# Optimization experiments

Hardware: AMD Instinct MI355X
Metric: run time of the kernel (lower is better)

The kernel has to match this reference:

```python
import jax, jax.numpy as jnp
import numpy as np

SEQ_LEN, BATCH, INPUT_SIZE, HIDDEN_SIZE = 512, 256, 256, 1024
ALPHA = 10.0 / 100.0  # dt / tau


def setup_inputs() -> dict:
    key = jax.random.key(0)
    k1, k2, k3, k4, k5 = jax.random.split(key, 5)
    s_in = 1.0 / np.sqrt(INPUT_SIZE)
    s_hh = 1.0 / np.sqrt(HIDDEN_SIZE)
    return {
        "x": jax.random.normal(k1, (SEQ_LEN, BATCH, INPUT_SIZE), jnp.float32),
        "W_in": jax.random.uniform(k2, (HIDDEN_SIZE, INPUT_SIZE), jnp.float32, -s_in, s_in),
        "b_in": jax.random.uniform(k3, (HIDDEN_SIZE,), jnp.float32, -s_in, s_in),
        "W_hh": jax.random.uniform(k4, (HIDDEN_SIZE, HIDDEN_SIZE), jnp.float32, -s_hh, s_hh),
        "b_hh": jax.random.uniform(k5, (HIDDEN_SIZE,), jnp.float32, -s_hh, s_hh),
    }


def reference(x, W_in, b_in, W_hh, b_hh):
    # Precompute input projection for all steps as one batched GEMM: [T,B,H]
    inp_proj = jnp.einsum("tbi,hi->tbh", x, W_in) + b_in

    def step(hidden, u_t):
        h_new = jax.nn.relu(u_t + hidden @ W_hh.T + b_hh)
        h_new = hidden * (1.0 - ALPHA) + h_new * ALPHA
        return h_new, h_new

    h0 = jnp.zeros((x.shape[1], W_hh.shape[0]), x.dtype)
    hidden, output = jax.lax.scan(step, h0, inp_proj)
    return output, hidden
```

## Files before the change

kernel.cpp:

```cpp
#include <hip/hip_runtime.h>
#include <hip/hip_bf16.h>
#include <stdint.h>
#include <stddef.h>

#define T_LEN 512
#define B_SZ  256
#define I_SZ  256
#define H_SZ  1024
#define NGRP  16

typedef __attribute__((ext_vector_type(8))) short bf16x8;
typedef __attribute__((ext_vector_type(4))) float f32x4;
typedef __attribute__((ext_vector_type(4))) unsigned int u32x4;
typedef unsigned short u16;
typedef unsigned int   u32;
typedef unsigned long long u64;

__device__ inline u16 f2bf(float f) {
  union { float f; u32 u; } x; x.f = f;
  u32 r = x.u + 0x7fffu + ((x.u >> 16) & 1u);
  return (u16)(r >> 16);
}
__device__ inline u32 bf2pk(u32 a, u32 b) {
  u32 ra = (a + 0x7fffu + ((a >> 16) & 1u)) >> 16;
  u32 rb = (b + 0x7fffu + ((b >> 16) & 1u)) >> 16;
  return ra | (rb << 16);
}

#define PIN8(B, i) asm volatile("" : "+v"(B[i]), "+v"(B[i+1]), "+v"(B[i+2]), \
    "+v"(B[i+3]), "+v"(B[i+4]), "+v"(B[i+5]), "+v"(B[i+6]), "+v"(B[i+7]))
#define PIN32(B) do { PIN8(B,0); PIN8(B,8); PIN8(B,16); PIN8(B,24); } while (0)

struct GCnt { u32 v; u32 pad[31]; };

__global__ __launch_bounds__(256) void cvt_kernel(const float* __restrict__ src,
                                                  u16* __restrict__ dst, int n) {
  int stride = gridDim.x * blockDim.x * 4;
  for (int i = (blockIdx.x * blockDim.x + threadIdx.x) * 4; i < n; i += stride) {
    float4 v = *reinterpret_cast<const float4*>(src + i);
    ushort4 o;
    o.x = f2bf(v.x); o.y = f2bf(v.y); o.z = f2bf(v.z); o.w = f2bf(v.w);
    *reinterpret_cast<ushort4*>(dst + i) = o;
  }
}

__global__ __launch_bounds__(256, 1) void rnn_persistent(
    const float* __restrict__ x, const u16* __restrict__ Win,
    const u16* __restrict__ Whh, const float* __restrict__ b_in,
    const float* __restrict__ b_hh, float* __restrict__ out,
    u16* __restrict__ hb0, u16* __restrict__ hb1, GCnt* __restrict__ cnts) {
  __shared__ __align__(16) u16 As[16 * 1024];
  __shared__ __align__(16) u16 Xs[2][16 * 256];

  const int b   = blockIdx.x;
  const int mg  = ((b & 7) << 1) | ((b >> 3) & 1);
  const int ng  = b >> 4;
  const int bm0 = mg * 16;
  const int bn0 = ng * 64;
  const int tid = threadIdx.x, lane = tid & 63, wid = tid >> 6;
  const int rl  = lane & 15, kq = lane >> 4;

  u32* cnt = &cnts[mg].v;

  const int wcol = bn0 + wid * 16 + rl;
  bf16x8 Breg[32];
#pragma unroll
  for (int kc = 0; kc < 32; ++kc)
    Breg[kc] = *reinterpret_cast<const bf16x8*>(Whh + (size_t)wcol * H_SZ + kc * 32 + kq * 8);
  bf16x8 Wreg[8];
#pragma unroll
  for (int kc = 0; kc < 8; ++kc)
    Wreg[kc] = *reinterpret_cast<const bf16x8*>(Win + (size_t)wcol * I_SZ + kc * 32 + kq * 8);
  PIN32(Breg);
  PIN8(Wreg, 0);

  const int row = bm0 + rl;
  const int c0  = bn0 + wid * 16 + kq * 4;
  float4 bsum;
#pragma unroll
  for (int r = 0; r < 4; ++r)
    (&bsum.x)[r] = b_in[c0 + r] + b_hh[c0 + r];

  float4 hprev = {0.f, 0.f, 0.f, 0.f};
  const char* Asb = (const char*)As;

  const int wb = (tid & 127) * 16;
  const int rb = tid >> 7;

  const int xc0 = tid * 2;

  {
    const float* xs = x;
#pragma unroll
    for (int j = 0; j < 2; ++j) {
      int c  = xc0 + j;
      int r_ = c >> 5;
      int cb = (c & 31) * 16;
      const float* src = xs + (size_t)(bm0 + r_) * I_SZ + (c & 31) * 8;
      float4 f0 = *reinterpret_cast<const float4*>(src);
      float4 f1 = *reinterpret_cast<const float4*>(src + 4);
      u32x4 v;
      v.x = (u32)f2bf(f0.x) | ((u32)f2bf(f0.y) << 16);
      v.y = (u32)f2bf(f0.z) | ((u32)f2bf(f0.w) << 16);
      v.z = (u32)f2bf(f1.x) | ((u32)f2bf(f1.y) << 16);
      v.w = (u32)f2bf(f1.z) | ((u32)f2bf(f1.w) << 16);
      int dst = r_ * 512 + (cb ^ ((r_ & 7) << 4));
      *reinterpret_cast<u32x4*>((char*)Xs[0] + dst) = v;
    }
  }
  __syncthreads();

  for (int t = 0; t < T_LEN; ++t) {
    const u16* hin = (t & 1) ? hb1 : hb0;
    u16* hout      = (t & 1) ? hb0 : hb1;

    PIN32(Breg);

    u32x4 sv[8];
    const char* hinb = (const char*)hin;
#pragma unroll
    for (int i = 0; i < 8; ++i) {
      int r_ = 2 * i + rb;
      const void* src = hinb + (size_t)(bm0 + r_) * 2048 + wb;
      asm volatile("global_load_dwordx4 %0, %1, off sc0 sc1"
                   : "=v"(sv[i]) : "v"(src) : "memory");
    }
    u32x4 xv[4];
    if (t < T_LEN - 1) {
      const float* xs = x + (size_t)(t + 1) * (B_SZ * I_SZ);
#pragma unroll
      for (int j = 0; j < 2; ++j) {
        int c = xc0 + j;
        int r_ = c >> 5;
        const void* src = xs + (size_t)(bm0 + r_) * I_SZ + (c & 31) * 8;
        asm volatile("global_load_dwordx4 %0, %1, off"
                     : "=v"(xv[2 * j]) : "v"(src) : "memory");
        asm volatile("global_load_dwordx4 %0, %1, off offset:16"
                     : "=v"(xv[2 * j + 1]) : "v"(src) : "memory");
      }
    }

    f32x4 acc2 = (f32x4){0.f, 0.f, 0.f, 0.f};
    {
      const char* Xb = (const char*)Xs[t & 1];
#pragma unroll
      for (int kc = 0; kc < 8; ++kc) {
        bf16x8 xa = *reinterpret_cast<const bf16x8*>(
            Xb + rl * 512 + ((kc * 64 + kq * 16) ^ ((rl & 7) << 4)));
        acc2 = __builtin_amdgcn_mfma_f32_16x16x32_bf16(Wreg[kc], xa, acc2, 0, 0, 0);
      }
    }

    if (t < T_LEN - 1) {
      asm volatile("s_waitcnt vmcnt(4)" ::: "memory");
    } else {
      asm volatile("s_waitcnt vmcnt(0)" ::: "memory");
    }
    __builtin_amdgcn_sched_barrier(0);
#pragma unroll
    for (int i = 0; i < 8; ++i) {
      int r_ = 2 * i + rb;
      int dst = r_ * 2048 + (wb ^ ((r_ & 7) << 4));
      *reinterpret_cast<u32x4*>((char*)As + dst) = sv[i];
    }
    __syncthreads();

    PIN32(Breg);

    f32x4 acc0 = (f32x4){0.f, 0.f, 0.f, 0.f};
    f32x4 acc1 = (f32x4){0.f, 0.f, 0.f, 0.f};
#pragma unroll
    for (int kc = 0; kc < 32; kc += 2) {
      bf16x8 a0 = *reinterpret_cast<const bf16x8*>(
          Asb + rl * 2048 + ((kc * 64 + kq * 16) ^ ((rl & 7) << 4)));
      acc0 = __builtin_amdgcn_mfma_f32_16x16x32_bf16(Breg[kc], a0, acc0, 0, 0, 0);
      bf16x8 a1 = *reinterpret_cast<const bf16x8*>(
          Asb + rl * 2048 + (((kc + 1) * 64 + kq * 16) ^ ((rl & 7) << 4)));
      acc1 = __builtin_amdgcn_mfma_f32_16x16x32_bf16(Breg[kc + 1], a1, acc1, 0, 0, 0);
    }

    float hv[4];
#pragma unroll
    for (int r = 0; r < 4; ++r) {
      float pre = acc0[r] + acc1[r] + acc2[r] + (&bsum.x)[r];
      float hn  = fmaxf(pre, 0.f);
      float h   = (&hprev.x)[r] * 0.9f + hn * 0.1f;
      (&hprev.x)[r] = h;
      hv[r] = h;
    }
    u32 lo = (u32)f2bf(hv[0]) | ((u32)f2bf(hv[1]) << 16);
    u32 hi = (u32)f2bf(hv[2]) | ((u32)f2bf(hv[3]) << 16);
    u64 pk = (u64)lo | ((u64)hi << 32);
    __hip_atomic_store(reinterpret_cast<u64*>(hout + (size_t)row * H_SZ + c0), pk,
                       __ATOMIC_RELAXED, __HIP_MEMORY_SCOPE_AGENT);

    __syncthreads();
    if (t < T_LEN - 1 && tid == 0)
      __hip_atomic_fetch_add(cnt, 1u, __ATOMIC_RELAXED, __HIP_MEMORY_SCOPE_AGENT);

    if (t < T_LEN - 1) {
      asm volatile("s_waitcnt vmcnt(0)" ::: "memory");
      __builtin_amdgcn_sched_barrier(0);
      char* Xw = (char*)Xs[(t + 1) & 1];
#pragma unroll
      for (int j = 0; j < 2; ++j) {
        int c  = xc0 + j;
        int r_ = c >> 5;
        int cb = (c & 31) * 16;
        u32x4 f0 = xv[2 * j], f1 = xv[2 * j + 1];
        u32x4 v;
        v.x = bf2pk(f0.x, f0.y);
        v.y = bf2pk(f0.z, f0.w);
        v.z = bf2pk(f1.x, f1.y);
        v.w = bf2pk(f1.z, f1.w);
        int dst = r_ * 512 + (cb ^ ((r_ & 7) << 4));
        *reinterpret_cast<u32x4*>(Xw + dst) = v;
      }
    }
    float4 ho = {hv[0], hv[1], hv[2], hv[3]};
    *reinterpret_cast<float4*>(out + (size_t)t * (B_SZ * H_SZ) +
                               (size_t)row * H_SZ + c0) = ho;
    if (t == T_LEN - 1)
      *reinterpret_cast<float4*>(out + (size_t)T_LEN * (B_SZ * H_SZ) +
                                 (size_t)row * H_SZ + c0) = ho;

    if (t < T_LEN - 1) {
      if (tid == 0) {
        const u32 tgt = (u32)(NGRP * (t + 1));
        while (__hip_atomic_load(cnt, __ATOMIC_RELAXED, __HIP_MEMORY_SCOPE_AGENT) < tgt) {
        }
      }
      __syncthreads();
      __builtin_amdgcn_sched_barrier(0);
    }
  }
}

extern "C" void kernel_launch(void* const* d_in, const int* in_sizes, int n_in,
                              void* d_out, int out_size, void* d_ws, size_t ws_size,
                              hipStream_t stream) {
  const float* x    = (const float*)d_in[0];
  const float* W_in = (const float*)d_in[1];
  const float* b_in = (const float*)d_in[2];
  const float* W_hh = (const float*)d_in[3];
  const float* b_hh = (const float*)d_in[4];
  float* out = (float*)d_out;

  const size_t off_wib = 0;
  const size_t off_whb = 524288;
  const size_t off_hb0 = 2621440;
  const size_t off_hb1 = 3145728;
  const size_t off_cnt = 3670016;
  const size_t need    = 3672064;
  if (ws_size < need) return;

  char* ws = (char*)d_ws;
  u16* wib  = (u16*)(ws + off_wib);
  u16* whb  = (u16*)(ws + off_whb);
  u16* hb0  = (u16*)(ws + off_hb0);
  u16* hb1  = (u16*)(ws + off_hb1);
  GCnt* cnts = (GCnt*)(ws + off_cnt);

  cvt_kernel<<<64,  256, 0, stream>>>(W_in, wib, H_SZ * I_SZ);
  cvt_kernel<<<256, 256, 0, stream>>>(W_hh, whb, H_SZ * H_SZ);
  hipMemsetAsync(hb0, 0, (size_t)B_SZ * H_SZ * sizeof(u16), stream);
  hipMemsetAsync(cnts, 0, NGRP * sizeof(GCnt), stream);

  rnn_persistent<<<256, 256, 0, stream>>>(x, wib, whb, b_in, b_hh,
                                          out, hb0, hb1, cnts);
}
```

Measured before the change: 1.209 ms.

## Replace counter barrier with epoch tag bits embedded in hidden-state data

Drops the per-group atomic counter barrier. Each 8-byte hidden-state store now carries a parity epoch bit in the sign bit of its first bf16, which is always free because the hidden state is non-negative. Consumers poll their own loaded chunks until every tag matches the expected epoch, then clear the bit before staging the values into LDS. This removes the fetch-add, the single-thread spin and two block barriers from each step's critical path. In exchange, all threads poll with sleeps and re-issue loads, and correctness depends on the stored values staying non-negative.

Result: slower. 2.497 ms (+106.5%).

```diff
diff --git a/kernel.cpp b/kernel.cpp
--- a/kernel.cpp
+++ b/kernel.cpp
@@ -7,7 +7,6 @@
 #define B_SZ  256
 #define I_SZ  256
 #define H_SZ  1024
-#define NGRP  16
 
 typedef __attribute__((ext_vector_type(8))) short bf16x8;
 typedef __attribute__((ext_vector_type(4))) float f32x4;
@@ -30,8 +29,6 @@
 #define PIN8(B, i) asm volatile("" : "+v"(B[i]), "+v"(B[i+1]), "+v"(B[i+2]), \
     "+v"(B[i+3]), "+v"(B[i+4]), "+v"(B[i+5]), "+v"(B[i+6]), "+v"(B[i+7]))
 #define PIN32(B) do { PIN8(B,0); PIN8(B,8); PIN8(B,16); PIN8(B,24); } while (0)
-
-struct GCnt { u32 v; u32 pad[31]; };
 
 __global__ __launch_bounds__(256) void cvt_kernel(const float* __restrict__ src,
                                                   u16* __restrict__ dst, int n) {
@@ -48,7 +45,7 @@
     const float* __restrict__ x, const u16* __restrict__ Win,
     const u16* __restrict__ Whh, const float* __restrict__ b_in,
     const float* __restrict__ b_hh, float* __restrict__ out,
-    u16* __restrict__ hb0, u16* __restrict__ hb1, GCnt* __restrict__ cnts) {
+    u16* __restrict__ hb0, u16* __restrict__ hb1) {
   __shared__ __align__(16) u16 As[16 * 1024];
   __shared__ __align__(16) u16 Xs[2][16 * 256];
 
@@ -59,8 +56,6 @@
   const int bn0 = ng * 64;
   const int tid = threadIdx.x, lane = tid & 63, wid = tid >> 6;
   const int rl  = lane & 15, kq = lane >> 4;
-
-  u32* cnt = &cnts[mg].v;
 
   const int wcol = bn0 + wid * 16 + rl;
   bf16x8 Breg[32];
@@ -116,27 +111,30 @@
 
     PIN32(Breg);
 
-    u32x4 sv[8];
+    u64 pv[16];
     const char* hinb = (const char*)hin;
 #pragma unroll
     for (int i = 0; i < 8; ++i) {
-      int r_ = 2 * i + rb;
-      const void* src = hinb + (size_t)(bm0 + r_) * 2048 + wb;
-      asm volatile("global_load_dwordx4 %0, %1, off sc0 sc1"
-                   : "=v"(sv[i]) : "v"(src) : "memory");
-    }
-    u32x4 xv[4];
+      const u64* p = reinterpret_cast<const u64*>(
+          hinb + (size_t)(bm0 + 2 * i + rb) * 2048 + wb);
+      pv[2 * i]     = __hip_atomic_load(p,     __ATOMIC_RELAXED, __HIP_MEMORY_SCOPE_AGENT);
+      pv[2 * i + 1] = __hip_atomic_load(p + 1, __ATOMIC_RELAXED, __HIP_MEMORY_SCOPE_AGENT);
+    }
+
+    float4 xf0a, xf0b, xf1a, xf1b;
     if (t < T_LEN - 1) {
       const float* xs = x + (size_t)(t + 1) * (B_SZ * I_SZ);
-#pragma unroll
-      for (int j = 0; j < 2; ++j) {
-        int c = xc0 + j;
-        int r_ = c >> 5;
-        const void* src = xs + (size_t)(bm0 + r_) * I_SZ + (c & 31) * 8;
-        asm volatile("global_load_dwordx4 %0, %1, off"
-                     : "=v"(xv[2 * j]) : "v"(src) : "memory");
-        asm volatile("global_load_dwordx4 %0, %1, off offset:16"
-                     : "=v"(xv[2 * j + 1]) : "v"(src) : "memory");
+      {
+        int c = xc0, r_ = c >> 5;
+        const float* src = xs + (size_t)(bm0 + r_) * I_SZ + (c & 31) * 8;
+        xf0a = *reinterpret_cast<const float4*>(src);
+        xf0b = *reinterpret_cast<const float4*>(src + 4);
+      }
+      {
+        int c = xc0 + 1, r_ = c >> 5;
+        const float* src = xs + (size_t)(bm0 + r_) * I_SZ + (c & 31) * 8;
+        xf1a = *reinterpret_cast<const float4*>(src);
+        xf1b = *reinterpret_cast<const float4*>(src + 4);
       }
     }
 
@@ -151,17 +149,32 @@
       }
     }
 
-    if (t < T_LEN - 1) {
-      asm volatile("s_waitcnt vmcnt(4)" ::: "memory");
-    } else {
-      asm volatile("s_waitcnt vmcnt(0)" ::: "memory");
-    }
-    __builtin_amdgcn_sched_barrier(0);
+    const u64 want = ((u64)((t >> 1) & 1)) << 15;
+    for (;;) {
+      u64 bad = 0;
+#pragma unroll
+      for (int i = 0; i < 16; ++i) bad |= (pv[i] ^ want) & 0x8000ull;
+      if (bad == 0) break;
+      __builtin_amdgcn_s_sleep(1);
+#pragma unroll
+      for (int i = 0; i < 8; ++i) {
+        const u64* p = reinterpret_cast<const u64*>(
+            hinb + (size_t)(bm0 + 2 * i + rb) * 2048 + wb);
+        pv[2 * i]     = __hip_atomic_load(p,     __ATOMIC_RELAXED, __HIP_MEMORY_SCOPE_AGENT);
+        pv[2 * i + 1] = __hip_atomic_load(p + 1, __ATOMIC_RELAXED, __HIP_MEMORY_SCOPE_AGENT);
+      }
+    }
+
 #pragma unroll
     for (int i = 0; i < 8; ++i) {
       int r_ = 2 * i + rb;
+      u64 a = pv[2 * i]     & ~0x8000ull;
+      u64 c = pv[2 * i + 1] & ~0x8000ull;
+      u32x4 v;
+      v.x = (u32)a; v.y = (u32)(a >> 32);
+      v.z = (u32)c; v.w = (u32)(c >> 32);
       int dst = r_ * 2048 + (wb ^ ((r_ & 7) << 4));
-      *reinterpret_cast<u32x4*>((char*)As + dst) = sv[i];
+      *reinterpret_cast<u32x4*>((char*)As + dst) = v;
     }
     __syncthreads();
 
@@ -188,35 +201,15 @@
       (&hprev.x)[r] = h;
       hv[r] = h;
     }
-    u32 lo = (u32)f2bf(hv[0]) | ((u32)f2bf(hv[1]) << 16);
-    u32 hi = (u32)f2bf(hv[2]) | ((u32)f2bf(hv[3]) << 16);
-    u64 pk = (u64)lo | ((u64)hi << 32);
-    __hip_atomic_store(reinterpret_cast<u64*>(hout + (size_t)row * H_SZ + c0), pk,
-                       __ATOMIC_RELAXED, __HIP_MEMORY_SCOPE_AGENT);
-
-    __syncthreads();
-    if (t < T_LEN - 1 && tid == 0)
-      __hip_atomic_fetch_add(cnt, 1u, __ATOMIC_RELAXED, __HIP_MEMORY_SCOPE_AGENT);
-
     if (t < T_LEN - 1) {
-      asm volatile("s_waitcnt vmcnt(0)" ::: "memory");
-      __builtin_amdgcn_sched_barrier(0);
-      char* Xw = (char*)Xs[(t + 1) & 1];
-#pragma unroll
-      for (int j = 0; j < 2; ++j) {
-        int c  = xc0 + j;
-        int r_ = c >> 5;
-        int cb = (c & 31) * 16;
-        u32x4 f0 = xv[2 * j], f1 = xv[2 * j + 1];
-        u32x4 v;
-        v.x = bf2pk(f0.x, f0.y);
-        v.y = bf2pk(f0.z, f0.w);
-        v.z = bf2pk(f1.x, f1.y);
-        v.w = bf2pk(f1.z, f1.w);
-        int dst = r_ * 512 + (cb ^ ((r_ & 7) << 4));
-        *reinterpret_cast<u32x4*>(Xw + dst) = v;
-      }
-    }
+      u32 lo = (u32)f2bf(hv[0]) | ((u32)f2bf(hv[1]) << 16);
+      u32 hi = (u32)f2bf(hv[2]) | ((u32)f2bf(hv[3]) << 16);
+      lo |= ((u32)(((t + 1) >> 1) & 1)) << 15;
+      u64 pk = (u64)lo | ((u64)hi << 32);
+      __hip_atomic_store(reinterpret_cast<u64*>(hout + (size_t)row * H_SZ + c0),
+                         pk, __ATOMIC_RELAXED, __HIP_MEMORY_SCOPE_AGENT);
+    }
+
     float4 ho = {hv[0], hv[1], hv[2], hv[3]};
     *reinterpret_cast<float4*>(out + (size_t)t * (B_SZ * H_SZ) +
                                (size_t)row * H_SZ + c0) = ho;
@@ -225,14 +218,28 @@
                                  (size_t)row * H_SZ + c0) = ho;
 
     if (t < T_LEN - 1) {
-      if (tid == 0) {
-        const u32 tgt = (u32)(NGRP * (t + 1));
-        while (__hip_atomic_load(cnt, __ATOMIC_RELAXED, __HIP_MEMORY_SCOPE_AGENT) < tgt) {
-        }
-      }
-      __syncthreads();
-      __builtin_amdgcn_sched_barrier(0);
-    }
+      char* Xw = (char*)Xs[(t + 1) & 1];
+      union { float4 f; u32x4 u; } a0u, a1u, b0u, b1u;
+      a0u.f = xf0a; a1u.f = xf0b; b0u.f = xf1a; b1u.f = xf1b;
+      {
+        int c = xc0, r_ = c >> 5, cb = (c & 31) * 16;
+        u32x4 v;
+        v.x = bf2pk(a0u.u.x, a0u.u.y); v.y = bf2pk(a0u.u.z, a0u.u.w);
+        v.z = bf2pk(a1u.u.x, a1u.u.y); v.w = bf2pk(a1u.u.z, a1u.u.w);
+        int dst = r_ * 512 + (cb ^ ((r_ & 7) << 4));
+        *reinterpret_cast<u32x4*>(Xw + dst) = v;
+      }
+      {
+        int c = xc0 + 1, r_ = c >> 5, cb = (c & 31) * 16;
+        u32x4 v;
+        v.x = bf2pk(b0u.u.x, b0u.u.y); v.y = bf2pk(b0u.u.z, b0u.u.w);
+        v.z = bf2pk(b1u.u.x, b1u.u.y); v.w = bf2pk(b1u.u.z, b1u.u.w);
+        int dst = r_ * 512 + (cb ^ ((r_ & 7) << 4));
+        *reinterpret_cast<u32x4*>(Xw + dst) = v;
+      }
+    }
+
+    __syncthreads();
   }
 }
 
@@ -250,22 +257,19 @@
   const size_t off_whb = 524288;
   const size_t off_hb0 = 2621440;
   const size_t off_hb1 = 3145728;
-  const size_t off_cnt = 3670016;
-  const size_t need    = 3672064;
+  const size_t need    = 3670016;
   if (ws_size < need) return;
 
   char* ws = (char*)d_ws;
-  u16* wib  = (u16*)(ws + off_wib);
-  u16* whb  = (u16*)(ws + off_whb);
-  u16* hb0  = (u16*)(ws + off_hb0);
-  u16* hb1  = (u16*)(ws + off_hb1);
-  GCnt* cnts = (GCnt*)(ws + off_cnt);
+  u16* wib = (u16*)(ws + off_wib);
+  u16* whb = (u16*)(ws + off_whb);
+  u16* hb0 = (u16*)(ws + off_hb0);
+  u16* hb1 = (u16*)(ws + off_hb1);
 
   cvt_kernel<<<64,  256, 0, stream>>>(W_in, wib, H_SZ * I_SZ);
   cvt_kernel<<<256, 256, 0, stream>>>(W_hh, whb, H_SZ * H_SZ);
   hipMemsetAsync(hb0, 0, (size_t)B_SZ * H_SZ * sizeof(u16), stream);
-  hipMemsetAsync(cnts, 0, NGRP * sizeof(GCnt), stream);
 
   rnn_persistent<<<256, 256, 0, stream>>>(x, wib, whb, b_in, b_hh,
-                                          out, hb0, hb1, cnts);
-}
+                                          out, hb0, hb1);
+}
```
